# Optimization experiments

Hardware: AMD Instinct MI355X
Metric: run time of the kernel (lower is better)

The kernel has to match this reference:

```python
import jax, jax.numpy as jnp
import numpy as np

N_QUBITS = 8

# Quantum circuit math: starting from |0...0>, apply RX(x_i) then RY(theta_i) on each
# wire independently (product state preserved). Exact PauliZ expectation per wire:
#   RX(x)|0> = cos(x/2)|0> - i sin(x/2)|1>;  after RY(t):
#   <Z> = cos(x) * cos(t)
# This is the exact closed form of the full state-vector simulation the torch module runs.

def setup_inputs() -> dict:
    key = jax.random.key(0)
    k1, k2, k3, k4 = jax.random.split(key, 4)
    B, S, D, F = 4, 4096, 1024, 4096
    x = jax.random.normal(k1, (B, S, D), dtype=jnp.float32)
    theta = jax.random.normal(k2, (N_QUBITS,), dtype=jnp.float32)
    W1 = jax.random.normal(k3, (F, N_QUBITS), dtype=jnp.float32) * (1.0 / np.sqrt(N_QUBITS))
    W2 = jax.random.normal(k4, (D, F), dtype=jnp.float32) * (1.0 / np.sqrt(F))
    return {"x": x, "theta": theta, "W1": W1, "W2": W2}


def reference(x, theta, W1, W2):
    # Encoder only reads the first n_qubits features of each token.
    z = jnp.cos(x[..., :N_QUBITS]) * jnp.cos(theta)          # [B, S, Q] PauliZ expectations
    h = jax.nn.relu(jnp.einsum('bsq,fq->bsf', z, W1))        # [B, S, ffn_dim]
    return jnp.einsum('bsf,df->bsd', h, W2)                  # [B, S, embed_dim]
```

## Files before the change

kernel.cpp:

```cpp
#include <hip/hip_runtime.h>
#include <hip/hip_bf16.h>
#include <math.h>


using f32x4  = __attribute__((ext_vector_type(4))) float;
using bf16x8 = __attribute__((ext_vector_type(8))) short;
using i32x4  = __attribute__((ext_vector_type(4))) int;
using u32x2  = __attribute__((ext_vector_type(2))) unsigned int;

#define M_TOT 16384
#define N_TOT 1024
#define K_TOT 4096
#define BM 128
#define BN 128
#define BK 64

static const size_t H_BYTES   = (size_t)M_TOT * K_TOT * 2;
static const size_t W2B_BYTES = (size_t)N_TOT * K_TOT * 2;
static const size_t Z_BYTES   = (size_t)M_TOT * 8 * 4;
static const size_t WS_NEED   = H_BYTES + W2B_BYTES + Z_BYTES;

#define TILE_BYTES (128 * 64 * 2)
#define SWZ(row, bytecol) ((bytecol) ^ (((row) & 7) << 4))

#define GLD16(gp, lp) __builtin_amdgcn_global_load_lds( \
    (const __attribute__((address_space(1))) unsigned int*)(const void*)(gp), \
    (__attribute__((address_space(3))) unsigned int*)(void*)(lp), 16, 0, 0)

static __device__ inline unsigned short f2bf(float f) {
    __hip_bfloat16 b = __float2bfloat16(f);
    unsigned short u;
    __builtin_memcpy(&u, &b, 2);
    return u;
}

__global__ __launch_bounds__(256)
void k_z(const float* __restrict__ x, const float* __restrict__ theta,
         float* __restrict__ z)
{
    const int m = blockIdx.x * 256 + threadIdx.x;
    const float* xp = x + (size_t)m * 1024;
    f32x4 a = *reinterpret_cast<const f32x4*>(xp);
    f32x4 b = *reinterpret_cast<const f32x4*>(xp + 4);
    f32x4 o0, o1;
    #pragma unroll
    for (int q = 0; q < 4; ++q) {
        o0[q] = cosf(a[q]) * cosf(theta[q]);
        o1[q] = cosf(b[q]) * cosf(theta[q + 4]);
    }
    *reinterpret_cast<f32x4*>(z + (size_t)m * 8)     = o0;
    *reinterpret_cast<f32x4*>(z + (size_t)m * 8 + 4) = o1;
}

__global__ __launch_bounds__(256)
void k_h(const float* __restrict__ z, const float* __restrict__ W1,
         unsigned short* __restrict__ hws)
{
    __shared__ float sZ[128 * 8];
    __shared__ float sW[128 * 8];
    const int bx = blockIdx.x;
    const int by = blockIdx.y;
    const int tid = threadIdx.x;

    *reinterpret_cast<f32x4*>(&sZ[tid * 4]) =
        *reinterpret_cast<const f32x4*>(z + (size_t)bx * 1024 + tid * 4);
    *reinterpret_cast<f32x4*>(&sW[tid * 4]) =
        *reinterpret_cast<const f32x4*>(W1 + (size_t)by * 1024 + tid * 4);
    __syncthreads();

    const int tm = tid >> 4;
    const int tk = tid & 15;

    f32x4 w1a[8], w1b[8];
    #pragma unroll
    for (int kk = 0; kk < 8; ++kk) {
        w1a[kk] = *reinterpret_cast<const f32x4*>(&sW[(tk * 8 + kk) * 8]);
        w1b[kk] = *reinterpret_cast<const f32x4*>(&sW[(tk * 8 + kk) * 8 + 4]);
    }

    const int kt    = by * 2 + (tk >> 3);
    const int kcolb = (tk & 7) * 16;
    unsigned short* tbase = hws + ((size_t)bx * 64 + kt) * (TILE_BYTES / 2);

    #pragma unroll
    for (int i = 0; i < 8; ++i) {
        const int row = tm * 8 + i;
        f32x4 za = *reinterpret_cast<const f32x4*>(&sZ[row * 8]);
        f32x4 zb = *reinterpret_cast<const f32x4*>(&sZ[row * 8 + 4]);
        unsigned hu[8];
        #pragma unroll
        for (int kk = 0; kk < 8; ++kk) {
            float h = 0.f;
            #pragma unroll
            for (int q = 0; q < 4; ++q) {
                h = fmaf(za[q], w1a[kk][q], h);
                h = fmaf(zb[q], w1b[kk][q], h);
            }
            hu[kk] = (unsigned)f2bf(fmaxf(h, 0.f));
        }
        i32x4 pk;
        pk[0] = (int)(hu[0] | (hu[1] << 16));
        pk[1] = (int)(hu[2] | (hu[3] << 16));
        pk[2] = (int)(hu[4] | (hu[5] << 16));
        pk[3] = (int)(hu[6] | (hu[7] << 16));
        char* dst = (char*)tbase + row * 128 + SWZ(row, kcolb);
        *reinterpret_cast<i32x4*>(dst) = pk;
    }
}

__global__ __launch_bounds__(256)
void k_w2(const float* __restrict__ W2, unsigned short* __restrict__ w2ws)
{
    const int gt = blockIdx.x * 256 + threadIdx.x;
    const int n  = gt >> 9;
    const int k8 = gt & 511;
    const float* p = W2 + (size_t)n * K_TOT + k8 * 8;
    f32x4 a = *reinterpret_cast<const f32x4*>(p);
    f32x4 b = *reinterpret_cast<const f32x4*>(p + 4);
    i32x4 pk;
    pk[0] = (int)((unsigned)f2bf(a[0]) | ((unsigned)f2bf(a[1]) << 16));
    pk[1] = (int)((unsigned)f2bf(a[2]) | ((unsigned)f2bf(a[3]) << 16));
    pk[2] = (int)((unsigned)f2bf(b[0]) | ((unsigned)f2bf(b[1]) << 16));
    pk[3] = (int)((unsigned)f2bf(b[2]) | ((unsigned)f2bf(b[3]) << 16));
    const int nt = n >> 7, row = n & 127, kt = k8 >> 3, kcolb = (k8 & 7) * 16;
    char* dst = (char*)(w2ws + ((size_t)nt * 64 + kt) * (TILE_BYTES / 2))
              + row * 128 + SWZ(row, kcolb);
    *reinterpret_cast<i32x4*>(dst) = pk;
}

__global__ __launch_bounds__(256, 4)
void k_gemm(const unsigned short* __restrict__ hws,
            const unsigned short* __restrict__ w2ws,
            float* __restrict__ out)
{
    __shared__ __align__(16) unsigned short sA[BM * BK];
    __shared__ __align__(16) unsigned short sB[BN * BK];

    const int tid  = threadIdx.x;
    const int lane = tid & 63;
    const int wave = tid >> 6;
    const int mt = blockIdx.x;
    const int nt = blockIdx.y;

    const char* atile0 = (const char*)hws  + (size_t)mt * 64 * TILE_BYTES;
    const char* btile0 = (const char*)w2ws + (size_t)nt * 64 * TILE_BYTES;

    f32x4 acc[4][4];
    #pragma unroll
    for (int i = 0; i < 4; ++i)
        #pragma unroll
        for (int j = 0; j < 4; ++j)
            acc[i][j] = {0.f, 0.f, 0.f, 0.f};

    const int wr   = (wave >> 1) * 64;
    const int wc   = (wave & 1) * 64;
    const int l16  = lane & 15;
    const int lk8b = (lane >> 4) * 16;
    const int ou   = wave * 1024 + lane * 16;
    const int ol   = wave * 1024;

    for (int ks = 0; ks < 64; ++ks) {
        const char* ga = atile0 + (size_t)ks * TILE_BYTES;
        const char* gb = btile0 + (size_t)ks * TILE_BYTES;
        #pragma unroll
        for (int c = 0; c < 4; ++c)
            GLD16(ga + c * 4096 + ou, (char*)sA + c * 4096 + ol);
        #pragma unroll
        for (int c = 0; c < 4; ++c)
            GLD16(gb + c * 4096 + ou, (char*)sB + c * 4096 + ol);
        __syncthreads();

        #pragma unroll
        for (int s = 0; s < 2; ++s) {
            bf16x8 af[4], bfr[4];
            #pragma unroll
            for (int i = 0; i < 4; ++i) {
                const int row = wr + i * 16 + l16;
                af[i] = *reinterpret_cast<const bf16x8*>(
                    (const char*)sA + row * 128 + SWZ(row, s * 64 + lk8b));
            }
            #pragma unroll
            for (int j = 0; j < 4; ++j) {
                const int row = wc + j * 16 + l16;
                bfr[j] = *reinterpret_cast<const bf16x8*>(
                    (const char*)sB + row * 128 + SWZ(row, s * 64 + lk8b));
            }
            #pragma unroll
            for (int i = 0; i < 4; ++i)
                #pragma unroll
                for (int j = 0; j < 4; ++j)
                    acc[i][j] = __builtin_amdgcn_mfma_f32_16x16x32_bf16(af[i], bfr[j], acc[i][j], 0, 0, 0);
        }
        __syncthreads();
    }

    const int orow0 = mt * BM + wr + (lane >> 4) * 4;
    const int ocol0 = nt * BN + wc + l16;
    #pragma unroll
    for (int i = 0; i < 4; ++i)
        #pragma unroll
        for (int j = 0; j < 4; ++j)
            #pragma unroll
            for (int jj = 0; jj < 4; ++jj)
                out[(size_t)(orow0 + i * 16 + jj) * N_TOT + (ocol0 + j * 16)] = acc[i][j][jj];
}

__global__ __launch_bounds__(256, 3)
void qffn_fused(const float* __restrict__ x, const float* __restrict__ theta,
                const float* __restrict__ W1, const float* __restrict__ W2,
                float* __restrict__ out)
{
    __shared__ __align__(16) unsigned short sA[BM * BK];
    __shared__ __align__(16) unsigned short sB[BN * BK];

    const int tid  = threadIdx.x;
    const int lane = tid & 63;
    const int wave = tid >> 6;
    const int m0 = blockIdx.x * BM;
    const int n0 = blockIdx.y * BN;

    const int arow = tid & 127;
    float zc[8];
    {
        const float* xp = x + (size_t)(m0 + arow) * 1024;
        f32x4 x0 = *reinterpret_cast<const f32x4*>(xp);
        f32x4 x1 = *reinterpret_cast<const f32x4*>(xp + 4);
        #pragma unroll
        for (int q = 0; q < 4; ++q) {
            zc[q]     = cosf(x0[q]) * cosf(theta[q]);
            zc[q + 4] = cosf(x1[q]) * cosf(theta[q + 4]);
        }
    }

    f32x4 acc[4][4];
    #pragma unroll
    for (int i = 0; i < 4; ++i)
        #pragma unroll
        for (int j = 0; j < 4; ++j)
            acc[i][j] = {0.f, 0.f, 0.f, 0.f};

    const int wr  = (wave >> 1) * 64;
    const int wc  = (wave & 1) * 64;
    const int l16 = lane & 15;
    const int lk8 = (lane >> 4) * 8;

    for (int k0 = 0; k0 < K_TOT; k0 += BK) {
        #pragma unroll
        for (int g = 0; g < 4; ++g) {
            const int cg  = (tid >> 7) + 2 * g;
            const int cgu = __builtin_amdgcn_readfirstlane(cg);
            const float* w1p = W1 + (size_t)(k0 + cgu * 8) * 8;
            i32x4 pk;
            #pragma unroll
            for (int p = 0; p < 4; ++p) {
                float h0 = 0.f, h1 = 0.f;
                #pragma unroll
                for (int q = 0; q < 8; ++q) {
                    h0 = fmaf(zc[q], w1p[(2 * p) * 8 + q], h0);
                    h1 = fmaf(zc[q], w1p[(2 * p + 1) * 8 + q], h1);
                }
                pk[p] = (int)(((unsigned)f2bf(fmaxf(h0, 0.f))) |
                              (((unsigned)f2bf(fmaxf(h1, 0.f))) << 16));
            }
            const int off = (arow * 64 + cg * 8) ^ ((arow & 7) << 3);
            *reinterpret_cast<i32x4*>(&sA[off]) = pk;
        }
        {
            const int fi = tid & 15;
            const int rb = tid >> 4;
            #pragma unroll
            for (int r = 0; r < 8; ++r) {
                const int row = rb + r * 16;
                f32x4 v = *(reinterpret_cast<const f32x4*>(W2 + (size_t)(n0 + row) * K_TOT + k0) + fi);
                u32x2 pk;
                pk[0] = (unsigned)f2bf(v[0]) | ((unsigned)f2bf(v[1]) << 16);
                pk[1] = (unsigned)f2bf(v[2]) | ((unsigned)f2bf(v[3]) << 16);
                const int off = (row * 64 + fi * 4) ^ ((row & 7) << 3);
                *reinterpret_cast<u32x2*>(&sB[off]) = pk;
            }
        }
        __syncthreads();

        #pragma unroll
        for (int s = 0; s < 2; ++s) {
            bf16x8 af[4], bfr[4];
            #pragma unroll
            for (int i = 0; i < 4; ++i) {
                const int row = wr + i * 16 + l16;
                const int off = (row * 64 + s * 32 + lk8) ^ ((row & 7) << 3);
                af[i] = *reinterpret_cast<const bf16x8*>(&sA[off]);
            }
            #pragma unroll
            for (int j = 0; j < 4; ++j) {
                const int row = wc + j * 16 + l16;
                const int off = (row * 64 + s * 32 + lk8) ^ ((row & 7) << 3);
                bfr[j] = *reinterpret_cast<const bf16x8*>(&sB[off]);
            }
            #pragma unroll
            for (int i = 0; i < 4; ++i)
                #pragma unroll
                for (int j = 0; j < 4; ++j)
                    acc[i][j] = __builtin_amdgcn_mfma_f32_16x16x32_bf16(af[i], bfr[j], acc[i][j], 0, 0, 0);
        }
        __syncthreads();
    }

    const int orow0 = m0 + wr + (lane >> 4) * 4;
    const int ocol0 = n0 + wc + l16;
    #pragma unroll
    for (int i = 0; i < 4; ++i)
        #pragma unroll
        for (int j = 0; j < 4; ++j)
            #pragma unroll
            for (int jj = 0; jj < 4; ++jj)
                out[(size_t)(orow0 + i * 16 + jj) * N_TOT + (ocol0 + j * 16)] = acc[i][j][jj];
}

extern "C" void kernel_launch(void* const* d_in, const int* in_sizes, int n_in,
                              void* d_out, int out_size, void* d_ws, size_t ws_size,
                              hipStream_t stream) {
    const float* x     = (const float*)d_in[0];
    const float* theta = (const float*)d_in[1];
    const float* W1    = (const float*)d_in[2];
    const float* W2    = (const float*)d_in[3];
    float* out = (float*)d_out;

    if (ws_size >= WS_NEED) {
        unsigned short* hws  = (unsigned short*)d_ws;
        unsigned short* w2ws = (unsigned short*)((char*)d_ws + H_BYTES);
        float*          zws  = (float*)((char*)d_ws + H_BYTES + W2B_BYTES);

        k_z<<<dim3(M_TOT / 256), dim3(256), 0, stream>>>(x, theta, zws);
        k_h<<<dim3(M_TOT / 128, K_TOT / 128), dim3(256), 0, stream>>>(zws, W1, hws);
        k_w2<<<dim3((N_TOT * K_TOT / 8) / 256), dim3(256), 0, stream>>>(W2, w2ws);
        k_gemm<<<dim3(M_TOT / BM, N_TOT / BN), dim3(256), 0, stream>>>(hws, w2ws, out);
    } else {
        qffn_fused<<<dim3(M_TOT / BM, N_TOT / BN), dim3(256), 0, stream>>>(x, theta, W1, W2, out);
    }
}
```

Baseline: 174.0 us.

## Enlarge GEMM tiles to 256x256 with 4-stage LDS pipeline and fuse z into k_h

The main GEMM moves from 128x128 tiles with BK=64 and a single LDS buffer to 256x256 tiles with 512 threads. It uses BK=32 k-tiles held in a four-deep ring of LDS buffers, filled by asynchronous global-to-LDS loads issued between MFMA groups, with explicit vmcnt waits and s_setprio. The workspace layouts for H and W2 are changed to 32-wide k-tiles with a new swizzle. The separate cos kernel is folded into k_h, which removes one launch and the z round trip through memory. The larger tiles cut redundant global traffic and hide load latency, at the cost of 128KB of LDS per block and higher register pressure.

```diff
diff --git a/kernel.cpp b/kernel.cpp
--- a/kernel.cpp
+++ b/kernel.cpp
@@ -6,22 +6,18 @@
 using f32x4  = __attribute__((ext_vector_type(4))) float;
 using bf16x8 = __attribute__((ext_vector_type(8))) short;
 using i32x4  = __attribute__((ext_vector_type(4))) int;
-using u32x2  = __attribute__((ext_vector_type(2))) unsigned int;
 
 #define M_TOT 16384
 #define N_TOT 1024
 #define K_TOT 4096
-#define BM 128
-#define BN 128
-#define BK 64
+#define NKT   128
+#define TILEB 16384
 
 static const size_t H_BYTES   = (size_t)M_TOT * K_TOT * 2;
 static const size_t W2B_BYTES = (size_t)N_TOT * K_TOT * 2;
-static const size_t Z_BYTES   = (size_t)M_TOT * 8 * 4;
-static const size_t WS_NEED   = H_BYTES + W2B_BYTES + Z_BYTES;
-
-#define TILE_BYTES (128 * 64 * 2)
-#define SWZ(row, bytecol) ((bytecol) ^ (((row) & 7) << 4))
+static const size_t WS_NEED   = H_BYTES + W2B_BYTES;
+
+#define SWZ32(row, bytecol) ((bytecol) ^ ((((row) >> 1) & 3) << 4))
 
 #define GLD16(gp, lp) __builtin_amdgcn_global_load_lds( \
     (const __attribute__((address_space(1))) unsigned int*)(const void*)(gp), \
@@ -35,35 +31,25 @@
 }
 
 __global__ __launch_bounds__(256)
-void k_z(const float* __restrict__ x, const float* __restrict__ theta,
-         float* __restrict__ z)
+void k_h(const float* __restrict__ x, const float* __restrict__ theta,
+         const float* __restrict__ W1, char* __restrict__ hws)
 {
-    const int m = blockIdx.x * 256 + threadIdx.x;
-    const float* xp = x + (size_t)m * 1024;
-    f32x4 a = *reinterpret_cast<const f32x4*>(xp);
-    f32x4 b = *reinterpret_cast<const f32x4*>(xp + 4);
-    f32x4 o0, o1;
-    #pragma unroll
-    for (int q = 0; q < 4; ++q) {
-        o0[q] = cosf(a[q]) * cosf(theta[q]);
-        o1[q] = cosf(b[q]) * cosf(theta[q + 4]);
-    }
-    *reinterpret_cast<f32x4*>(z + (size_t)m * 8)     = o0;
-    *reinterpret_cast<f32x4*>(z + (size_t)m * 8 + 4) = o1;
-}
-
-__global__ __launch_bounds__(256)
-void k_h(const float* __restrict__ z, const float* __restrict__ W1,
-         unsigned short* __restrict__ hws)
-{
-    __shared__ float sZ[128 * 8];
+    __shared__ float sZ[256 * 8];
     __shared__ float sW[128 * 8];
-    const int bx = blockIdx.x;
-    const int by = blockIdx.y;
     const int tid = threadIdx.x;
-
-    *reinterpret_cast<f32x4*>(&sZ[tid * 4]) =
-        *reinterpret_cast<const f32x4*>(z + (size_t)bx * 1024 + tid * 4);
+    const int bx  = blockIdx.x;
+    const int by  = blockIdx.y;
+
+    {
+        const float* xp = x + ((size_t)bx * 256 + tid) * 1024;
+        f32x4 a = *reinterpret_cast<const f32x4*>(xp);
+        f32x4 b = *reinterpret_cast<const f32x4*>(xp + 4);
+        #pragma unroll
+        for (int q = 0; q < 4; ++q) {
+            sZ[tid * 8 + q]     = cosf(a[q]) * cosf(theta[q]);
+            sZ[tid * 8 + 4 + q] = cosf(b[q]) * cosf(theta[q + 4]);
+        }
+    }
     *reinterpret_cast<f32x4*>(&sW[tid * 4]) =
         *reinterpret_cast<const f32x4*>(W1 + (size_t)by * 1024 + tid * 4);
     __syncthreads();
@@ -71,20 +57,20 @@
     const int tm = tid >> 4;
     const int tk = tid & 15;
 
-    f32x4 w1a[8], w1b[8];
+    f32x4 wA[8], wB[8];
     #pragma unroll
     for (int kk = 0; kk < 8; ++kk) {
-        w1a[kk] = *reinterpret_cast<const f32x4*>(&sW[(tk * 8 + kk) * 8]);
-        w1b[kk] = *reinterpret_cast<const f32x4*>(&sW[(tk * 8 + kk) * 8 + 4]);
-    }
-
-    const int kt    = by * 2 + (tk >> 3);
-    const int kcolb = (tk & 7) * 16;
-    unsigned short* tbase = hws + ((size_t)bx * 64 + kt) * (TILE_BYTES / 2);
-
-    #pragma unroll
-    for (int i = 0; i < 8; ++i) {
-        const int row = tm * 8 + i;
+        wA[kk] = *reinterpret_cast<const f32x4*>(&sW[(tk * 8 + kk) * 8]);
+        wB[kk] = *reinterpret_cast<const f32x4*>(&sW[(tk * 8 + kk) * 8 + 4]);
+    }
+
+    const int kt    = by * 4 + (tk >> 2);
+    const int slotb = (tk & 3) * 16;
+    char* tb = hws + ((size_t)bx * NKT + kt) * TILEB;
+
+    #pragma unroll
+    for (int i = 0; i < 16; ++i) {
+        const int row = tm * 16 + i;
         f32x4 za = *reinterpret_cast<const f32x4*>(&sZ[row * 8]);
         f32x4 zb = *reinterpret_cast<const f32x4*>(&sZ[row * 8 + 4]);
         unsigned hu[8];
@@ -93,8 +79,8 @@
             float h = 0.f;
             #pragma unroll
             for (int q = 0; q < 4; ++q) {
-                h = fmaf(za[q], w1a[kk][q], h);
-                h = fmaf(zb[q], w1b[kk][q], h);
+                h = fmaf(za[q], wA[kk][q], h);
+                h = fmaf(zb[q], wB[kk][q], h);
             }
             hu[kk] = (unsigned)f2bf(fmaxf(h, 0.f));
         }
@@ -103,13 +89,12 @@
         pk[1] = (int)(hu[2] | (hu[3] << 16));
         pk[2] = (int)(hu[4] | (hu[5] << 16));
         pk[3] = (int)(hu[6] | (hu[7] << 16));
-        char* dst = (char*)tbase + row * 128 + SWZ(row, kcolb);
-        *reinterpret_cast<i32x4*>(dst) = pk;
+        *reinterpret_cast<i32x4*>(tb + row * 64 + SWZ32(row, slotb)) = pk;
     }
 }
 
 __global__ __launch_bounds__(256)
-void k_w2(const float* __restrict__ W2, unsigned short* __restrict__ w2ws)
+void k_w2(const float* __restrict__ W2, char* __restrict__ w2ws)
 {
     const int gt = blockIdx.x * 256 + threadIdx.x;
     const int n  = gt >> 9;
@@ -122,82 +107,126 @@
     pk[1] = (int)((unsigned)f2bf(a[2]) | ((unsigned)f2bf(a[3]) << 16));
     pk[2] = (int)((unsigned)f2bf(b[0]) | ((unsigned)f2bf(b[1]) << 16));
     pk[3] = (int)((unsigned)f2bf(b[2]) | ((unsigned)f2bf(b[3]) << 16));
-    const int nt = n >> 7, row = n & 127, kt = k8 >> 3, kcolb = (k8 & 7) * 16;
-    char* dst = (char*)(w2ws + ((size_t)nt * 64 + kt) * (TILE_BYTES / 2))
-              + row * 128 + SWZ(row, kcolb);
+    const int nt = n >> 8, row = n & 255, kt = k8 >> 2, slotb = (k8 & 3) * 16;
+    char* dst = w2ws + ((size_t)nt * NKT + kt) * TILEB + row * 64 + SWZ32(row, slotb);
     *reinterpret_cast<i32x4*>(dst) = pk;
 }
 
-__global__ __launch_bounds__(256, 4)
-void k_gemm(const unsigned short* __restrict__ hws,
-            const unsigned short* __restrict__ w2ws,
+
+#define KTILE_BODY(BUF, KT, DOSTAGE)                                              \
+    bf16x8 a[4], a2[4], b[4];                                                     \
+    _Pragma("unroll")                                                             \
+    for (int i = 0; i < 4; ++i)                                                   \
+        a[i] = *reinterpret_cast<const bf16x8*>(lds + (BUF) * 16384 + aoff[i]);   \
+    _Pragma("unroll")                                                             \
+    for (int j = 0; j < 4; ++j)                                                   \
+        b[j] = *reinterpret_cast<const bf16x8*>(lds + 65536 + (BUF) * 16384 + boff[j]); \
+    if (DOSTAGE) {                                                                \
+        const char* g = aT + (size_t)((KT) + 3) * TILEB;                          \
+        GLD16(g + tid * 16,        lds + (((BUF) + 3) & 3) * 16384 + wave * 1024);        \
+        GLD16(g + 8192 + tid * 16, lds + (((BUF) + 3) & 3) * 16384 + 8192 + wave * 1024); \
+    }                                                                             \
+    __builtin_amdgcn_s_setprio(1);                                                \
+    _Pragma("unroll")                                                             \
+    for (int i = 0; i < 4; ++i)                                                   \
+        _Pragma("unroll")                                                         \
+        for (int j = 0; j < 4; ++j)                                               \
+            acc[i][j] = __builtin_amdgcn_mfma_f32_16x16x32_bf16(a[i], b[j], acc[i][j], 0, 0, 0); \
+    __builtin_amdgcn_s_setprio(0);                                                \
+    _Pragma("unroll")                                                             \
+    for (int i = 0; i < 4; ++i)                                                   \
+        a2[i] = *reinterpret_cast<const bf16x8*>(lds + (BUF) * 16384 + aoff[i + 4]); \
+    if (DOSTAGE) {                                                                \
+        const char* g = bT + (size_t)((KT) + 3) * TILEB;                          \
+        GLD16(g + tid * 16,        lds + 65536 + (((BUF) + 3) & 3) * 16384 + wave * 1024);        \
+        GLD16(g + 8192 + tid * 16, lds + 65536 + (((BUF) + 3) & 3) * 16384 + 8192 + wave * 1024); \
+    }                                                                             \
+    __builtin_amdgcn_s_setprio(1);                                                \
+    _Pragma("unroll")                                                             \
+    for (int i = 0; i < 4; ++i)                                                   \
+        _Pragma("unroll")                                                         \
+        for (int j = 0; j < 4; ++j)                                               \
+            acc[i + 4][j] = __builtin_amdgcn_mfma_f32_16x16x32_bf16(a2[i], b[j], acc[i + 4][j], 0, 0, 0); \
+    __builtin_amdgcn_s_setprio(0);
+
+#define KTILE(BUF, KT, DOSTAGE, WN) do {                                          \
+    KTILE_BODY(BUF, KT, DOSTAGE)                                                  \
+    asm volatile("s_waitcnt vmcnt(" #WN ")" ::: "memory");                        \
+    __builtin_amdgcn_sched_barrier(0);                                            \
+    __builtin_amdgcn_s_barrier();                                                 \
+    __builtin_amdgcn_sched_barrier(0);                                            \
+} while (0)
+
+#define KTILE_LAST(BUF, KT) do { KTILE_BODY(BUF, KT, 0) } while (0)
+
+__global__ __launch_bounds__(512, 2)
+void k_gemm(const char* __restrict__ hws, const char* __restrict__ w2ws,
             float* __restrict__ out)
 {
-    __shared__ __align__(16) unsigned short sA[BM * BK];
-    __shared__ __align__(16) unsigned short sB[BN * BK];
+    __shared__ __align__(16) char lds[131072];
 
     const int tid  = threadIdx.x;
     const int lane = tid & 63;
     const int wave = tid >> 6;
+    const int wm = wave >> 2;
+    const int wn = wave & 3;
     const int mt = blockIdx.x;
     const int nt = blockIdx.y;
 
-    const char* atile0 = (const char*)hws  + (size_t)mt * 64 * TILE_BYTES;
-    const char* btile0 = (const char*)w2ws + (size_t)nt * 64 * TILE_BYTES;
-
-    f32x4 acc[4][4];
-    #pragma unroll
-    for (int i = 0; i < 4; ++i)
+    const char* aT = hws  + (size_t)mt * NKT * TILEB;
+    const char* bT = w2ws + (size_t)nt * NKT * TILEB;
+
+    const int l16 = lane & 15;
+    const int lkb = (lane >> 4) * 16;
+    int aoff[8], boff[4];
+    #pragma unroll
+    for (int i = 0; i < 8; ++i) {
+        const int row = wm * 128 + i * 16 + l16;
+        aoff[i] = row * 64 + SWZ32(row, lkb);
+    }
+    #pragma unroll
+    for (int j = 0; j < 4; ++j) {
+        const int row = wn * 64 + j * 16 + l16;
+        boff[j] = row * 64 + SWZ32(row, lkb);
+    }
+
+    f32x4 acc[8][4];
+    #pragma unroll
+    for (int i = 0; i < 8; ++i)
         #pragma unroll
         for (int j = 0; j < 4; ++j)
             acc[i][j] = {0.f, 0.f, 0.f, 0.f};
 
-    const int wr   = (wave >> 1) * 64;
-    const int wc   = (wave & 1) * 64;
-    const int l16  = lane & 15;
-    const int lk8b = (lane >> 4) * 16;
-    const int ou   = wave * 1024 + lane * 16;
-    const int ol   = wave * 1024;
-
-    for (int ks = 0; ks < 64; ++ks) {
-        const char* ga = atile0 + (size_t)ks * TILE_BYTES;
-        const char* gb = btile0 + (size_t)ks * TILE_BYTES;
-        #pragma unroll
-        for (int c = 0; c < 4; ++c)
-            GLD16(ga + c * 4096 + ou, (char*)sA + c * 4096 + ol);
-        #pragma unroll
-        for (int c = 0; c < 4; ++c)
-            GLD16(gb + c * 4096 + ou, (char*)sB + c * 4096 + ol);
-        __syncthreads();
-
-        #pragma unroll
-        for (int s = 0; s < 2; ++s) {
-            bf16x8 af[4], bfr[4];
-            #pragma unroll
-            for (int i = 0; i < 4; ++i) {
-                const int row = wr + i * 16 + l16;
-                af[i] = *reinterpret_cast<const bf16x8*>(
-                    (const char*)sA + row * 128 + SWZ(row, s * 64 + lk8b));
-            }
-            #pragma unroll
-            for (int j = 0; j < 4; ++j) {
-                const int row = wc + j * 16 + l16;
-                bfr[j] = *reinterpret_cast<const bf16x8*>(
-                    (const char*)sB + row * 128 + SWZ(row, s * 64 + lk8b));
-            }
-            #pragma unroll
-            for (int i = 0; i < 4; ++i)
-                #pragma unroll
-                for (int j = 0; j < 4; ++j)
-                    acc[i][j] = __builtin_amdgcn_mfma_f32_16x16x32_bf16(af[i], bfr[j], acc[i][j], 0, 0, 0);
-        }
-        __syncthreads();
-    }
-
-    const int orow0 = mt * BM + wr + (lane >> 4) * 4;
-    const int ocol0 = nt * BN + wc + l16;
-    #pragma unroll
-    for (int i = 0; i < 4; ++i)
+    #pragma unroll
+    for (int t = 0; t < 3; ++t) {
+        const char* ga = aT + (size_t)t * TILEB;
+        const char* gb = bT + (size_t)t * TILEB;
+        GLD16(ga + tid * 16,        lds + t * 16384 + wave * 1024);
+        GLD16(ga + 8192 + tid * 16, lds + t * 16384 + 8192 + wave * 1024);
+        GLD16(gb + tid * 16,        lds + 65536 + t * 16384 + wave * 1024);
+        GLD16(gb + 8192 + tid * 16, lds + 65536 + t * 16384 + 8192 + wave * 1024);
+    }
+    asm volatile("s_waitcnt vmcnt(8)" ::: "memory");
+    __builtin_amdgcn_sched_barrier(0);
+    __builtin_amdgcn_s_barrier();
+    __builtin_amdgcn_sched_barrier(0);
+
+    #pragma unroll 1
+    for (int t = 0; t < NKT - 4; t += 4) {
+        KTILE(0, t,     1, 8);
+        KTILE(1, t + 1, 1, 8);
+        KTILE(2, t + 2, 1, 8);
+        KTILE(3, t + 3, 1, 8);
+    }
+    KTILE(0, NKT - 4, 1, 8);
+    KTILE(1, NKT - 3, 0, 4);
+    KTILE(2, NKT - 2, 0, 0);
+    KTILE_LAST(3, NKT - 1);
+
+    const int orow0 = mt * 256 + wm * 128 + (lane >> 4) * 4;
+    const int ocol0 = nt * 256 + wn * 64 + l16;
+    #pragma unroll
+    for (int i = 0; i < 8; ++i)
         #pragma unroll
         for (int j = 0; j < 4; ++j)
             #pragma unroll
@@ -210,14 +239,14 @@
                 const float* __restrict__ W1, const float* __restrict__ W2,
                 float* __restrict__ out)
 {
-    __shared__ __align__(16) unsigned short sA[BM * BK];
-    __shared__ __align__(16) unsigned short sB[BN * BK];
+    __shared__ __align__(16) unsigned short sA[128 * 64];
+    __shared__ __align__(16) unsigned short sB[128 * 64];
 
     const int tid  = threadIdx.x;
     const int lane = tid & 63;
     const int wave = tid >> 6;
-    const int m0 = blockIdx.x * BM;
-    const int n0 = blockIdx.y * BN;
+    const int m0 = blockIdx.x * 128;
+    const int n0 = blockIdx.y * 128;
 
     const int arow = tid & 127;
     float zc[8];
@@ -244,7 +273,7 @@
     const int l16 = lane & 15;
     const int lk8 = (lane >> 4) * 8;
 
-    for (int k0 = 0; k0 < K_TOT; k0 += BK) {
+    for (int k0 = 0; k0 < K_TOT; k0 += 64) {
         #pragma unroll
         for (int g = 0; g < 4; ++g) {
             const int cg  = (tid >> 7) + 2 * g;
@@ -272,11 +301,11 @@
             for (int r = 0; r < 8; ++r) {
                 const int row = rb + r * 16;
                 f32x4 v = *(reinterpret_cast<const f32x4*>(W2 + (size_t)(n0 + row) * K_TOT + k0) + fi);
-                u32x2 pk;
-                pk[0] = (unsigned)f2bf(v[0]) | ((unsigned)f2bf(v[1]) << 16);
-                pk[1] = (unsigned)f2bf(v[2]) | ((unsigned)f2bf(v[3]) << 16);
+                unsigned p0 = (unsigned)f2bf(v[0]) | ((unsigned)f2bf(v[1]) << 16);
+                unsigned p1 = (unsigned)f2bf(v[2]) | ((unsigned)f2bf(v[3]) << 16);
                 const int off = (row * 64 + fi * 4) ^ ((row & 7) << 3);
-                *reinterpret_cast<u32x2*>(&sB[off]) = pk;
+                *reinterpret_cast<unsigned*>(&sB[off])     = p0;
+                *reinterpret_cast<unsigned*>(&sB[off + 2]) = p1;
             }
         }
         __syncthreads();
@@ -326,15 +355,13 @@
     float* out = (float*)d_out;
 
     if (ws_size >= WS_NEED) {
-        unsigned short* hws  = (unsigned short*)d_ws;
-        unsigned short* w2ws = (unsigned short*)((char*)d_ws + H_BYTES);
-        float*          zws  = (float*)((char*)d_ws + H_BYTES + W2B_BYTES);
-
-        k_z<<<dim3(M_TOT / 256), dim3(256), 0, stream>>>(x, theta, zws);
-        k_h<<<dim3(M_TOT / 128, K_TOT / 128), dim3(256), 0, stream>>>(zws, W1, hws);
+        char* hws  = (char*)d_ws;
+        char* w2ws = (char*)d_ws + H_BYTES;
+
+        k_h<<<dim3(M_TOT / 256, K_TOT / 128), dim3(256), 0, stream>>>(x, theta, W1, hws);
         k_w2<<<dim3((N_TOT * K_TOT / 8) / 256), dim3(256), 0, stream>>>(W2, w2ws);
-        k_gemm<<<dim3(M_TOT / BM, N_TOT / BN), dim3(256), 0, stream>>>(hws, w2ws, out);
+        k_gemm<<<dim3(M_TOT / 256, N_TOT / 256), dim3(512), 0, stream>>>(hws, w2ws, out);
     } else {
-        qffn_fused<<<dim3(M_TOT / BM, N_TOT / BN), dim3(256), 0, stream>>>(x, theta, W1, W2, out);
-    }
-}
+        qffn_fused<<<dim3(M_TOT / 128, N_TOT / 128), dim3(256), 0, stream>>>(x, theta, W1, W2, out);
+    }
+}
```

After: 146.2 us. 1.19x faster.
